# Kernel tuning notes

Measured on AMD Instinct MI355X. Metric: run time of the kernel, lower is better.

Reference implementation:

```python
import jax, jax.numpy as jnp
import numpy as np

G = 56          # voxel grid resolution per axis
N = 65536
K = 27          # 3x3x3 kernel offsets
C_IN = 128
C_OUT = 128


def _build_rulebook():
    """Submanifold conv rulebook: for each kernel offset, (input_row, output_row) pairs.

    Padded to P=N pairs per offset; invalid pairs use in_idx=0 and out_idx=N
    (a dummy output slot that is dropped), so shapes are static.
    """
    rng = np.random.default_rng(0)
    keys = np.sort(rng.choice(G ** 3, size=N, replace=False)).astype(np.int64)
    x = keys // (G * G)
    y = (keys // G) % G
    z = keys % G
    in_idx = np.zeros((K, N), dtype=np.int32)
    out_idx = np.full((K, N), N, dtype=np.int32)
    k = 0
    for dx in (-1, 0, 1):
        for dy in (-1, 0, 1):
            for dz in (-1, 0, 1):
                nx, ny, nz = x + dx, y + dy, z + dz
                valid = (nx >= 0) & (nx < G) & (ny >= 0) & (ny < G) & (nz >= 0) & (nz < G)
                nkey = (nx * G + ny) * G + nz
                pos = np.searchsorted(keys, np.clip(nkey, 0, G ** 3 - 1))
                pos = np.clip(pos, 0, N - 1)
                found = valid & (keys[pos] == nkey)
                cnt = int(found.sum())
                in_idx[k, :cnt] = pos[found]
                out_idx[k, :cnt] = np.nonzero(found)[0]
                k += 1
    return jnp.asarray(in_idx), jnp.asarray(out_idx)


def setup_inputs() -> dict:
    key = jax.random.key(0)
    k1, k2, k3 = jax.random.split(key, 3)
    fan_in = K * C_IN
    features = jax.random.normal(k1, (N, C_IN), dtype=jnp.float32)
    weight = jax.random.normal(k2, (K, C_IN, C_OUT), dtype=jnp.float32) * (1.0 / np.sqrt(fan_in))
    bias = jax.random.normal(k3, (C_OUT,), dtype=jnp.float32) * 0.01
    in_idx, out_idx = _build_rulebook()
    return {"features": features, "weight": weight, "bias": bias,
            "in_idx": in_idx, "out_idx": out_idx}


def reference(features, weight, bias, in_idx, out_idx):
    # gather: [K, P, C_in]
    gathered = features[in_idx]
    # per-offset GEMM: [K, P, C_out]
    contrib = jnp.einsum('kpc,kcd->kpd', gathered, weight)
    n = features.shape[0]
    c_out = weight.shape[-1]
    # scatter-accumulate into N real rows + 1 dummy row for padded pairs
    out = jnp.zeros((n + 1, c_out), dtype=features.dtype)
    out = out.at[out_idx.reshape(-1)].add(contrib.reshape(-1, c_out))
    return out[:n] + bias
```

## Files before the change

kernel.cpp:

```cpp
#include <hip/hip_runtime.h>
#include <hip/hip_bf16.h>
#include <stdint.h>

#define NV   65536
#define KOFF 27
#define CIN  128
#define COUT 128
#define NSEC (NV + 128)

typedef __bf16 bf16x8 __attribute__((ext_vector_type(8)));
typedef float  f32x4  __attribute__((ext_vector_type(4)));

__device__ __forceinline__ void async_copy16(void* lds, const void* g) {
    __builtin_amdgcn_global_load_lds(
        (const __attribute__((address_space(1))) void*)g,
        (__attribute__((address_space(3))) void*)lds,
        16, 0, 0);
}

#define JOB_A_BLOCKS 4097
#define JOB_B_BLOCKS 216
#define JOB_S_BLOCKS 1728

__global__ void k_prep_all(const float* __restrict__ f,
                           uint4* __restrict__ fb4,
                           const float* __restrict__ w,
                           uint4* __restrict__ wfrag4,
                           const int4* __restrict__ in4,
                           const int4* __restrict__ out4,
                           int* __restrict__ nbr) {
    const int b = blockIdx.x;
    const int t = threadIdx.x;
    if (b < JOB_A_BLOCKS) {
        int i = b * 256 + t;
        int total8  = (NV + 1) * CIN / 8;
        int nvalid8 = NV * CIN / 8;
        if (i >= total8) return;
        union { uint4 u; __hip_bfloat16 h[8]; } p;
        if (i < nvalid8) {
            const float4* f4 = (const float4*)f;
            float4 a = f4[i * 2];
            float4 c = f4[i * 2 + 1];
            p.h[0] = __float2bfloat16(a.x);
            p.h[1] = __float2bfloat16(a.y);
            p.h[2] = __float2bfloat16(a.z);
            p.h[3] = __float2bfloat16(a.w);
            p.h[4] = __float2bfloat16(c.x);
            p.h[5] = __float2bfloat16(c.y);
            p.h[6] = __float2bfloat16(c.z);
            p.h[7] = __float2bfloat16(c.w);
        } else {
            p.u = make_uint4(0, 0, 0, 0);
        }
        fb4[i] = p.u;
    } else if (b < JOB_A_BLOCKS + JOB_B_BLOCKS) {
        int c    = (b - JOB_A_BLOCKS) * 256 + t;
        int lane = c & 63;
        int nt   = (c >> 6) & 1;
        int ks   = (c >> 7) & 3;
        int wv   = (c >> 9) & 3;
        int k    = c >> 11;
        int cout = wv * 32 + nt * 16 + (lane & 15);
        int cin0 = ks * 32 + (lane >> 4) * 8;
        const float* wk = w + k * 16384;
        union { uint4 u; __hip_bfloat16 h[8]; } p;
        #pragma unroll
        for (int j = 0; j < 8; ++j)
            p.h[j] = __float2bfloat16(wk[(cin0 + j) * 128 + cout]);
        wfrag4[c] = p.u;
    } else {
        int i = (b - JOB_A_BLOCKS - JOB_B_BLOCKS) * 256 + t;
        int k = i >> 14;
        int4 ii = in4[i];
        int4 oo = out4[i];
        int* nb = nbr + (size_t)k * NSEC;
        auto POS = [](int o) {
            return (o >> 7) * 128 + (o & 15) * 8 + ((o >> 4) & 7);
        };
        nb[POS(oo.x)] = ii.x;
        nb[POS(oo.y)] = ii.y;
        nb[POS(oo.z)] = ii.z;
        nb[POS(oo.w)] = ii.w;
    }
}

__global__ __launch_bounds__(256, 2)
void sp_conv_main(const __hip_bfloat16* __restrict__ feats,
                  const uint4* __restrict__ wfrag,
                  const int* __restrict__ nbrt,
                  const float* __restrict__ bias,
                  float* __restrict__ out) {
    __shared__ unsigned char smem[65536];

    const int t   = threadIdx.x;
    const int bid = blockIdx.x;
    const int tile0 = ((bid & 7) * 64 + (bid >> 3)) * 128;

    const int w    = t >> 6;
    const int lane = t & 63;
    const int lr   = lane & 15;
    const int quad = lane >> 4;

    const int srow  = t >> 4;
    const int sbyte = ((t & 15) ^ srow) * 16;

    f32x4 acc[8][2] = {};

    const unsigned char* featsB = (const unsigned char*)feats;

    int  arows[8];
    uint4 bA[4][2], bB[4][2];

    auto NLOAD = [&](int k) {
        const int4* np = (const int4*)(nbrt + (size_t)k * NSEC + tile0 + srow * 8);
        int4 a0 = np[0];
        int4 a1 = np[1];
        arows[0] = a0.x; arows[1] = a0.y; arows[2] = a0.z; arows[3] = a0.w;
        arows[4] = a1.x; arows[5] = a1.y; arows[6] = a1.z; arows[7] = a1.w;
    };
    auto STAGE = [&](int sb) {
        #pragma unroll
        for (int i = 0; i < 8; ++i) {
            unsigned ar = min((unsigned)arows[i], (unsigned)NV);
            async_copy16(smem + sb + i * 4096 + t * 16,
                         featsB + (size_t)ar * 256 + sbyte);
        }
    };
    auto BLOAD = [&](const uint4* wfk, uint4 (&b)[4][2]) {
        #pragma unroll
        for (int ks = 0; ks < 4; ++ks)
            #pragma unroll
            for (int nt = 0; nt < 2; ++nt)
                b[ks][nt] = wfk[ks * 128 + nt * 64];
    };
    auto AFLOAD = [&](int rb, int ks, bf16x8 (&af)[8]) {
        #pragma unroll
        for (int mt = 0; mt < 8; ++mt)
            af[mt] = *(const bf16x8*)(smem + rb + (mt * 16 + lr) * 256 +
                                      (((ks * 4 + quad) ^ lr) * 16));
    };
    auto MFMA16 = [&](bf16x8 (&af)[8], uint4 (&b)[2]) {
        #pragma unroll
        for (int mt = 0; mt < 8; ++mt)
            #pragma unroll
            for (int nt = 0; nt < 2; ++nt)
                acc[mt][nt] = __builtin_amdgcn_mfma_f32_16x16x32_bf16(
                    af[mt], *(const bf16x8*)&b[nt], acc[mt][nt], 0, 0, 0);
    };

    NLOAD(0);
    STAGE(0);
    __builtin_amdgcn_sched_barrier(0);
    NLOAD(1);
    BLOAD(wfrag + w * 512 + lane, bA);
    asm volatile("s_waitcnt vmcnt(10)" ::: "memory");
    __builtin_amdgcn_s_barrier();
    __builtin_amdgcn_sched_barrier(0);

    auto ITER = [&](int k, int rb, uint4 (&buse)[4][2], uint4 (&bload)[4][2]) {
        STAGE(rb ^ 32768);
        __builtin_amdgcn_sched_barrier(0);
        NLOAD(min(k + 2, KOFF - 1));
        BLOAD(wfrag + (k + 1) * 2048 + w * 512 + lane, bload);
        #pragma unroll
        for (int ks = 0; ks < 4; ++ks) {
            bf16x8 af[8];
            AFLOAD(rb, ks, af);
            __builtin_amdgcn_s_setprio(1);
            MFMA16(af, buse[ks]);
            __builtin_amdgcn_s_setprio(0);
        }
        __builtin_amdgcn_sched_barrier(0);
        asm volatile("s_waitcnt vmcnt(10)" ::: "memory");
        __builtin_amdgcn_s_barrier();
        __builtin_amdgcn_sched_barrier(0);
    };

    #pragma unroll 1
    for (int kk = 0; kk < KOFF - 1; kk += 2) {
        ITER(kk,     0,     bA, bB);
        ITER(kk + 1, 32768, bB, bA);
    }

    #pragma unroll
    for (int ks = 0; ks < 4; ++ks) {
        bf16x8 af[8];
        AFLOAD(0, ks, af);
        MFMA16(af, bA[ks]);
    }

    const int n0w = w * 32;
    float bv[2];
    #pragma unroll
    for (int nt = 0; nt < 2; ++nt) bv[nt] = bias[n0w + nt * 16 + lr];

    #pragma unroll
    for (int mt = 0; mt < 8; ++mt) {
        #pragma unroll
        for (int nt = 0; nt < 2; ++nt) {
            #pragma unroll
            for (int r = 0; r < 4; ++r) {
                int grow = tile0 + mt * 16 + quad * 4 + r;
                out[(size_t)grow * COUT + n0w + nt * 16 + lr] =
                    acc[mt][nt][r] + bv[nt];
            }
        }
    }
}


extern "C" void kernel_launch(void* const* d_in, const int* in_sizes, int n_in,
                              void* d_out, int out_size, void* d_ws, size_t ws_size,
                              hipStream_t stream) {
    const float* features = (const float*)d_in[0];
    const float* weight   = (const float*)d_in[1];
    const float* bias     = (const float*)d_in[2];
    const int*   in_idx   = (const int*)d_in[3];
    const int*   out_idx  = (const int*)d_in[4];
    float* out = (float*)d_out;

    uint8_t* ws = (uint8_t*)d_ws;
    size_t off = 0;
    __hip_bfloat16* feats_bf = (__hip_bfloat16*)(ws + off);
    off += (size_t)(NV + 1) * CIN * 2;
    off = (off + 255) & ~(size_t)255;
    uint4* wfrag = (uint4*)(ws + off);
    off += (size_t)KOFF * CIN * COUT * 2;
    off = (off + 255) & ~(size_t)255;
    int* nbr = (int*)(ws + off);

    hipMemsetAsync(nbr, 0xFF, (size_t)KOFF * NSEC * 4, stream);

    k_prep_all<<<JOB_A_BLOCKS + JOB_B_BLOCKS + JOB_S_BLOCKS, 256, 0, stream>>>(
        features, (uint4*)feats_bf, weight, wfrag,
        (const int4*)in_idx, (const int4*)out_idx, nbr);

    sp_conv_main<<<NV / 128, 256, 0, stream>>>(feats_bf, wfrag, nbr, bias, out);
}
```

Before: 151.6 us.

## Switch warp tiling to 2x2 grid and stream weight fragments in halves

Each of the four waves now computes a 64x64 output sub-tile (2x2 wave grid) instead of a 128x32 strip, so each wave loads 4 A fragments and 4 B fragments per k-step. This halves the LDS A-fragment reads per wave while doubling the B fragments per wave. The double-buffered B registers are replaced by a single buffer that is refilled in two halves interleaved with the MFMA phases, cutting register pressure. This relies on the next offset's weight loads landing before they are consumed, and the vmcnt wait count is adjusted to match.

```diff
diff --git a/kernel.cpp b/kernel.cpp
--- a/kernel.cpp
+++ b/kernel.cpp
@@ -100,16 +100,18 @@
     const int lane = t & 63;
     const int lr   = lane & 15;
     const int quad = lane >> 4;
+    const int wr   = w >> 1;
+    const int wc   = w & 1;
 
     const int srow  = t >> 4;
     const int sbyte = ((t & 15) ^ srow) * 16;
 
-    f32x4 acc[8][2] = {};
+    f32x4 acc[4][4] = {};
 
     const unsigned char* featsB = (const unsigned char*)feats;
 
     int  arows[8];
-    uint4 bA[4][2], bB[4][2];
+    uint4 bcur[4][4];
 
     auto NLOAD = [&](int k) {
         const int4* np = (const int4*)(nbrt + (size_t)k * NSEC + tile0 + srow * 8);
@@ -126,24 +128,25 @@
                          featsB + (size_t)ar * 256 + sbyte);
         }
     };
-    auto BLOAD = [&](const uint4* wfk, uint4 (&b)[4][2]) {
-        #pragma unroll
-        for (int ks = 0; ks < 4; ++ks)
+    auto BLOAD2 = [&](const uint4* wfk, int ks0) {
+        #pragma unroll
+        for (int ks = 0; ks < 2; ++ks)
             #pragma unroll
-            for (int nt = 0; nt < 2; ++nt)
-                b[ks][nt] = wfk[ks * 128 + nt * 64];
-    };
-    auto AFLOAD = [&](int rb, int ks, bf16x8 (&af)[8]) {
-        #pragma unroll
-        for (int mt = 0; mt < 8; ++mt)
-            af[mt] = *(const bf16x8*)(smem + rb + (mt * 16 + lr) * 256 +
+            for (int nt = 0; nt < 4; ++nt)
+                bcur[ks0 + ks][nt] =
+                    wfk[(nt >> 1) * 512 + (nt & 1) * 64 + (ks0 + ks) * 128];
+    };
+    auto AFLOAD = [&](int rb, int ks, bf16x8 (&af)[4]) {
+        #pragma unroll
+        for (int mt = 0; mt < 4; ++mt)
+            af[mt] = *(const bf16x8*)(smem + rb + (wr * 64 + mt * 16 + lr) * 256 +
                                       (((ks * 4 + quad) ^ lr) * 16));
     };
-    auto MFMA16 = [&](bf16x8 (&af)[8], uint4 (&b)[2]) {
-        #pragma unroll
-        for (int mt = 0; mt < 8; ++mt)
+    auto MFMA16 = [&](bf16x8 (&af)[4], uint4 (&b)[4]) {
+        #pragma unroll
+        for (int mt = 0; mt < 4; ++mt)
             #pragma unroll
-            for (int nt = 0; nt < 2; ++nt)
+            for (int nt = 0; nt < 4; ++nt)
                 acc[mt][nt] = __builtin_amdgcn_mfma_f32_16x16x32_bf16(
                     af[mt], *(const bf16x8*)&b[nt], acc[mt][nt], 0, 0, 0);
     };
@@ -152,55 +155,73 @@
     STAGE(0);
     __builtin_amdgcn_sched_barrier(0);
     NLOAD(1);
-    BLOAD(wfrag + w * 512 + lane, bA);
-    asm volatile("s_waitcnt vmcnt(10)" ::: "memory");
+    {
+        const uint4* wf0 = wfrag + wc * 1024 + lane;
+        BLOAD2(wf0, 0);
+        BLOAD2(wf0, 2);
+    }
+    asm volatile("s_waitcnt vmcnt(18)" ::: "memory");
     __builtin_amdgcn_s_barrier();
     __builtin_amdgcn_sched_barrier(0);
 
-    auto ITER = [&](int k, int rb, uint4 (&buse)[4][2], uint4 (&bload)[4][2]) {
+    auto ITER = [&](int k, int rb) {
+        const uint4* wfn = wfrag + (min(k + 1, KOFF - 1)) * 2048 + wc * 1024 + lane;
         STAGE(rb ^ 32768);
         __builtin_amdgcn_sched_barrier(0);
         NLOAD(min(k + 2, KOFF - 1));
-        BLOAD(wfrag + (k + 1) * 2048 + w * 512 + lane, bload);
-        #pragma unroll
-        for (int ks = 0; ks < 4; ++ks) {
-            bf16x8 af[8];
+        __builtin_amdgcn_sched_barrier(0);
+        #pragma unroll
+        for (int ks = 0; ks < 2; ++ks) {
+            bf16x8 af[4];
             AFLOAD(rb, ks, af);
             __builtin_amdgcn_s_setprio(1);
-            MFMA16(af, buse[ks]);
+            MFMA16(af, bcur[ks]);
             __builtin_amdgcn_s_setprio(0);
         }
         __builtin_amdgcn_sched_barrier(0);
-        asm volatile("s_waitcnt vmcnt(10)" ::: "memory");
+        BLOAD2(wfn, 0);
+        __builtin_amdgcn_sched_barrier(0);
+        #pragma unroll
+        for (int ks = 2; ks < 4; ++ks) {
+            bf16x8 af[4];
+            AFLOAD(rb, ks, af);
+            __builtin_amdgcn_s_setprio(1);
+            MFMA16(af, bcur[ks]);
+            __builtin_amdgcn_s_setprio(0);
+        }
+        __builtin_amdgcn_sched_barrier(0);
+        BLOAD2(wfn, 2);
+        __builtin_amdgcn_sched_barrier(0);
+        asm volatile("s_waitcnt vmcnt(18)" ::: "memory");
         __builtin_amdgcn_s_barrier();
         __builtin_amdgcn_sched_barrier(0);
     };
 
     #pragma unroll 1
     for (int kk = 0; kk < KOFF - 1; kk += 2) {
-        ITER(kk,     0,     bA, bB);
-        ITER(kk + 1, 32768, bB, bA);
+        ITER(kk,     0);
+        ITER(kk + 1, 32768);
     }
 
     #pragma unroll
     for (int ks = 0; ks < 4; ++ks) {
-        bf16x8 af[8];
+        bf16x8 af[4];
         AFLOAD(0, ks, af);
-        MFMA16(af, bA[ks]);
-    }
-
-    const int n0w = w * 32;
-    float bv[2];
+        MFMA16(af, bcur[ks]);
+    }
+
+    const int n0w = wc * 64;
+    float bv[4];
     #pragma unroll
-    for (int nt = 0; nt < 2; ++nt) bv[nt] = bias[n0w + nt * 16 + lr];
+    for (int nt = 0; nt < 4; ++nt) bv[nt] = bias[n0w + nt * 16 + lr];
 
     #pragma unroll
-    for (int mt = 0; mt < 8; ++mt) {
-        #pragma unroll
-        for (int nt = 0; nt < 2; ++nt) {
+    for (int mt = 0; mt < 4; ++mt) {
+        #pragma unroll
+        for (int nt = 0; nt < 4; ++nt) {
             #pragma unroll
             for (int r = 0; r < 4; ++r) {
-                int grow = tile0 + mt * 16 + quad * 4 + r;
+                int grow = tile0 + wr * 64 + mt * 16 + quad * 4 + r;
                 out[(size_t)grow * COUT + n0w + nt * 16 + lr] =
                     acc[mt][nt][r] + bv[nt];
             }
```

Result: no change. 153.4 us (+1.2%).

## Add dedicated producer wavefront for async gather staging of feature rows

Applied to the files above, without the earlier changes.

Adds a fifth wavefront per block that loads the neighbor indices and issues all async global-to-LDS gathers for the next offset. The four compute wavefronts now only load weight fragments and run MFMAs, synchronising with the producer through block barriers. The neighbor table is now written in natural row order instead of a permuted order, and the LDS swizzle is moved into the producer's chunk XOR. The goal is to take gather-issue work and vmcnt waits off the MFMA waves, at the cost of a larger block, serialized readlane address generation in one wave, and a full vmcnt(0) wait each step.

```diff
diff --git a/kernel.cpp b/kernel.cpp
--- a/kernel.cpp
+++ b/kernel.cpp
@@ -74,20 +74,17 @@
         int4 ii = in4[i];
         int4 oo = out4[i];
         int* nb = nbr + (size_t)k * NSEC;
-        auto POS = [](int o) {
-            return (o >> 7) * 128 + (o & 15) * 8 + ((o >> 4) & 7);
-        };
-        nb[POS(oo.x)] = ii.x;
-        nb[POS(oo.y)] = ii.y;
-        nb[POS(oo.z)] = ii.z;
-        nb[POS(oo.w)] = ii.w;
-    }
-}
-
-__global__ __launch_bounds__(256, 2)
+        nb[oo.x] = ii.x;
+        nb[oo.y] = ii.y;
+        nb[oo.z] = ii.z;
+        nb[oo.w] = ii.w;
+    }
+}
+
+__global__ __launch_bounds__(320, 2)
 void sp_conv_main(const __hip_bfloat16* __restrict__ feats,
                   const uint4* __restrict__ wfrag,
-                  const int* __restrict__ nbrt,
+                  const int* __restrict__ nbrp,
                   const float* __restrict__ bias,
                   float* __restrict__ out) {
     __shared__ unsigned char smem[65536];
@@ -101,31 +98,49 @@
     const int lr   = lane & 15;
     const int quad = lane >> 4;
 
-    const int srow  = t >> 4;
-    const int sbyte = ((t & 15) ^ srow) * 16;
+    const unsigned char* featsB = (const unsigned char*)feats;
+
+    if (w == 4) {
+        auto NBRLOAD = [&](int k) {
+            int4 v = make_int4(NV, NV, NV, NV);
+            if (lane < 32)
+                v = *(const int4*)(nbrp + (size_t)k * NSEC + tile0 + lane * 4);
+            return v;
+        };
+        auto PSTAGE = [&](int sb, int4 nv) {
+            #pragma unroll
+            for (int j = 0; j < 32; ++j) {
+                unsigned r0 = min((unsigned)__builtin_amdgcn_readlane(nv.x, j), (unsigned)NV);
+                unsigned r1 = min((unsigned)__builtin_amdgcn_readlane(nv.y, j), (unsigned)NV);
+                unsigned r2 = min((unsigned)__builtin_amdgcn_readlane(nv.z, j), (unsigned)NV);
+                unsigned r3 = min((unsigned)__builtin_amdgcn_readlane(nv.w, j), (unsigned)NV);
+                unsigned ar = quad == 0 ? r0 : quad == 1 ? r1 : quad == 2 ? r2 : r3;
+                unsigned chunk = (unsigned)(lane & 15) ^ ((unsigned)(j & 3) * 4 + (unsigned)quad);
+                async_copy16(smem + sb + j * 1024 + lane * 16,
+                             featsB + (size_t)ar * 256 + chunk * 16);
+            }
+        };
+
+        int4 nvC = NBRLOAD(0);
+        int4 nvN = NBRLOAD(1);
+        PSTAGE(0, nvC);
+        asm volatile("s_waitcnt vmcnt(0)" ::: "memory");
+        __builtin_amdgcn_s_barrier();
+        nvC = nvN;
+        #pragma unroll 1
+        for (int k = 0; k < KOFF - 1; ++k) {
+            nvN = NBRLOAD(min(k + 2, KOFF - 1));
+            PSTAGE(((k + 1) & 1) * 32768, nvC);
+            asm volatile("s_waitcnt vmcnt(0)" ::: "memory");
+            __builtin_amdgcn_s_barrier();
+            nvC = nvN;
+        }
+        return;
+    }
 
     f32x4 acc[8][2] = {};
-
-    const unsigned char* featsB = (const unsigned char*)feats;
-
-    int  arows[8];
     uint4 bA[4][2], bB[4][2];
 
-    auto NLOAD = [&](int k) {
-        const int4* np = (const int4*)(nbrt + (size_t)k * NSEC + tile0 + srow * 8);
-        int4 a0 = np[0];
-        int4 a1 = np[1];
-        arows[0] = a0.x; arows[1] = a0.y; arows[2] = a0.z; arows[3] = a0.w;
-        arows[4] = a1.x; arows[5] = a1.y; arows[6] = a1.z; arows[7] = a1.w;
-    };
-    auto STAGE = [&](int sb) {
-        #pragma unroll
-        for (int i = 0; i < 8; ++i) {
-            unsigned ar = min((unsigned)arows[i], (unsigned)NV);
-            async_copy16(smem + sb + i * 4096 + t * 16,
-                         featsB + (size_t)ar * 256 + sbyte);
-        }
-    };
     auto BLOAD = [&](const uint4* wfk, uint4 (&b)[4][2]) {
         #pragma unroll
         for (int ks = 0; ks < 4; ++ks)
@@ -147,47 +162,28 @@
                 acc[mt][nt] = __builtin_amdgcn_mfma_f32_16x16x32_bf16(
                     af[mt], *(const bf16x8*)&b[nt], acc[mt][nt], 0, 0, 0);
     };
-
-    NLOAD(0);
-    STAGE(0);
-    __builtin_amdgcn_sched_barrier(0);
-    NLOAD(1);
-    BLOAD(wfrag + w * 512 + lane, bA);
-    asm volatile("s_waitcnt vmcnt(10)" ::: "memory");
-    __builtin_amdgcn_s_barrier();
-    __builtin_amdgcn_sched_barrier(0);
-
-    auto ITER = [&](int k, int rb, uint4 (&buse)[4][2], uint4 (&bload)[4][2]) {
-        STAGE(rb ^ 32768);
-        __builtin_amdgcn_sched_barrier(0);
-        NLOAD(min(k + 2, KOFF - 1));
-        BLOAD(wfrag + (k + 1) * 2048 + w * 512 + lane, bload);
+    auto COMPUTE = [&](int rb, uint4 (&buse)[4][2]) {
         #pragma unroll
         for (int ks = 0; ks < 4; ++ks) {
             bf16x8 af[8];
             AFLOAD(rb, ks, af);
-            __builtin_amdgcn_s_setprio(1);
             MFMA16(af, buse[ks]);
-            __builtin_amdgcn_s_setprio(0);
-        }
-        __builtin_amdgcn_sched_barrier(0);
-        asm volatile("s_waitcnt vmcnt(10)" ::: "memory");
-        __builtin_amdgcn_s_barrier();
-        __builtin_amdgcn_sched_barrier(0);
-    };
+        }
+    };
+
+    BLOAD(wfrag + w * 512 + lane, bA);
+    __builtin_amdgcn_s_barrier();
 
     #pragma unroll 1
     for (int kk = 0; kk < KOFF - 1; kk += 2) {
-        ITER(kk,     0,     bA, bB);
-        ITER(kk + 1, 32768, bB, bA);
-    }
-
-    #pragma unroll
-    for (int ks = 0; ks < 4; ++ks) {
-        bf16x8 af[8];
-        AFLOAD(0, ks, af);
-        MFMA16(af, bA[ks]);
-    }
+        BLOAD(wfrag + (kk + 1) * 2048 + w * 512 + lane, bB);
+        COMPUTE(0, bA);
+        __builtin_amdgcn_s_barrier();
+        BLOAD(wfrag + (kk + 2) * 2048 + w * 512 + lane, bA);
+        COMPUTE(32768, bB);
+        __builtin_amdgcn_s_barrier();
+    }
+    COMPUTE(0, bA);
 
     const int n0w = w * 32;
     float bv[2];
@@ -235,5 +231,5 @@
         features, (uint4*)feats_bf, weight, wfrag,
         (const int4*)in_idx, (const int4*)out_idx, nbr);
 
-    sp_conv_main<<<NV / 128, 256, 0, stream>>>(feats_bf, wfrag, nbr, bias, out);
-}
+    sp_conv_main<<<NV / 128, 320, 0, stream>>>(feats_bf, wfrag, nbr, bias, out);
+}
```

New measurement: 256.2 us. +69.0%, slower.

## Switch to 32x32x16 MFMA with 2x2 wave tiling and single weight buffer

Applied to the files above, without the earlier changes.

Replaces the 16x16x32 bf16 MFMA with 32x32x16 MFMA. The four waves now split the 128x128 tile 2x2 (64 rows by 64 cols each) instead of 128 rows by 32 cols per wave, so each wave reads a quarter of the A tile from LDS. The weight fragment layout in the prep kernel is rearranged to match. The double-buffered weight registers become one buffer refilled slice by slice right after each use, which cuts register pressure but can leave MFMAs waiting on global loads.

```diff
diff --git a/kernel.cpp b/kernel.cpp
--- a/kernel.cpp
+++ b/kernel.cpp
@@ -9,7 +9,7 @@
 #define NSEC (NV + 128)
 
 typedef __bf16 bf16x8 __attribute__((ext_vector_type(8)));
-typedef float  f32x4  __attribute__((ext_vector_type(4)));
+typedef float  f32x16 __attribute__((ext_vector_type(16)));
 
 __device__ __forceinline__ void async_copy16(void* lds, const void* g) {
     __builtin_amdgcn_global_load_lds(
@@ -56,12 +56,12 @@
     } else if (b < JOB_A_BLOCKS + JOB_B_BLOCKS) {
         int c    = (b - JOB_A_BLOCKS) * 256 + t;
         int lane = c & 63;
-        int nt   = (c >> 6) & 1;
-        int ks   = (c >> 7) & 3;
-        int wv   = (c >> 9) & 3;
+        int ks   = (c >> 6) & 7;
+        int nb   = (c >> 9) & 1;
+        int wc   = (c >> 10) & 1;
         int k    = c >> 11;
-        int cout = wv * 32 + nt * 16 + (lane & 15);
-        int cin0 = ks * 32 + (lane >> 4) * 8;
+        int cout = wc * 64 + nb * 32 + (lane & 31);
+        int cin0 = ks * 16 + (lane >> 5) * 8;
         const float* wk = w + k * 16384;
         union { uint4 u; __hip_bfloat16 h[8]; } p;
         #pragma unroll
@@ -98,18 +98,23 @@
 
     const int w    = t >> 6;
     const int lane = t & 63;
-    const int lr   = lane & 15;
-    const int quad = lane >> 4;
+    const int wr   = w >> 1;
+    const int wc   = w & 1;
+    const int l31  = lane & 31;
+    const int part = lane >> 5;
+    const int x15  = lane & 15;
 
     const int srow  = t >> 4;
     const int sbyte = ((t & 15) ^ srow) * 16;
 
-    f32x4 acc[8][2] = {};
+    const int rowb0 = (wr * 64 + l31) * 256;
+    const int rowb1 = rowb0 + 8192;
+
+    f32x16 acc[2][2] = {};
+    uint4  bcur[8][2];
 
     const unsigned char* featsB = (const unsigned char*)feats;
-
-    int  arows[8];
-    uint4 bA[4][2], bB[4][2];
+    int arows[8];
 
     auto NLOAD = [&](int k) {
         const int4* np = (const int4*)(nbrt + (size_t)k * NSEC + tile0 + srow * 8);
@@ -126,83 +131,84 @@
                          featsB + (size_t)ar * 256 + sbyte);
         }
     };
-    auto BLOAD = [&](const uint4* wfk, uint4 (&b)[4][2]) {
-        #pragma unroll
-        for (int ks = 0; ks < 4; ++ks)
-            #pragma unroll
-            for (int nt = 0; nt < 2; ++nt)
-                b[ks][nt] = wfk[ks * 128 + nt * 64];
-    };
-    auto AFLOAD = [&](int rb, int ks, bf16x8 (&af)[8]) {
-        #pragma unroll
-        for (int mt = 0; mt < 8; ++mt)
-            af[mt] = *(const bf16x8*)(smem + rb + (mt * 16 + lr) * 256 +
-                                      (((ks * 4 + quad) ^ lr) * 16));
-    };
-    auto MFMA16 = [&](bf16x8 (&af)[8], uint4 (&b)[2]) {
-        #pragma unroll
-        for (int mt = 0; mt < 8; ++mt)
-            #pragma unroll
-            for (int nt = 0; nt < 2; ++nt)
-                acc[mt][nt] = __builtin_amdgcn_mfma_f32_16x16x32_bf16(
-                    af[mt], *(const bf16x8*)&b[nt], acc[mt][nt], 0, 0, 0);
-    };
 
     NLOAD(0);
     STAGE(0);
     __builtin_amdgcn_sched_barrier(0);
     NLOAD(1);
-    BLOAD(wfrag + w * 512 + lane, bA);
-    asm volatile("s_waitcnt vmcnt(10)" ::: "memory");
+    {
+        const uint4* wf0 = wfrag + wc * 1024 + lane;
+        #pragma unroll
+        for (int ks = 0; ks < 8; ++ks) {
+            bcur[ks][0] = wf0[ks * 64];
+            bcur[ks][1] = wf0[ks * 64 + 512];
+        }
+    }
+    asm volatile("s_waitcnt vmcnt(18)" ::: "memory");
     __builtin_amdgcn_s_barrier();
     __builtin_amdgcn_sched_barrier(0);
 
-    auto ITER = [&](int k, int rb, uint4 (&buse)[4][2], uint4 (&bload)[4][2]) {
+    auto ITER = [&](int k, int rb) {
         STAGE(rb ^ 32768);
         __builtin_amdgcn_sched_barrier(0);
         NLOAD(min(k + 2, KOFF - 1));
-        BLOAD(wfrag + (k + 1) * 2048 + w * 512 + lane, bload);
-        #pragma unroll
-        for (int ks = 0; ks < 4; ++ks) {
-            bf16x8 af[8];
-            AFLOAD(rb, ks, af);
-            __builtin_amdgcn_s_setprio(1);
-            MFMA16(af, buse[ks]);
-            __builtin_amdgcn_s_setprio(0);
-        }
-        __builtin_amdgcn_sched_barrier(0);
-        asm volatile("s_waitcnt vmcnt(10)" ::: "memory");
+        const uint4* wfn = wfrag + (k + 1) * 2048 + wc * 1024 + lane;
+        #pragma unroll
+        for (int ks = 0; ks < 8; ++ks) {
+            bf16x8 af0 = *(const bf16x8*)(smem + rb + rowb0 +
+                                          (((ks * 2 + part) ^ x15) << 4));
+            bf16x8 af1 = *(const bf16x8*)(smem + rb + rowb1 +
+                                          (((ks * 2 + part) ^ x15) << 4));
+            acc[0][0] = __builtin_amdgcn_mfma_f32_32x32x16_bf16(
+                af0, *(const bf16x8*)&bcur[ks][0], acc[0][0], 0, 0, 0);
+            acc[0][1] = __builtin_amdgcn_mfma_f32_32x32x16_bf16(
+                af0, *(const bf16x8*)&bcur[ks][1], acc[0][1], 0, 0, 0);
+            acc[1][0] = __builtin_amdgcn_mfma_f32_32x32x16_bf16(
+                af1, *(const bf16x8*)&bcur[ks][0], acc[1][0], 0, 0, 0);
+            acc[1][1] = __builtin_amdgcn_mfma_f32_32x32x16_bf16(
+                af1, *(const bf16x8*)&bcur[ks][1], acc[1][1], 0, 0, 0);
+            bcur[ks][0] = wfn[ks * 64];
+            bcur[ks][1] = wfn[ks * 64 + 512];
+        }
+        asm volatile("s_waitcnt vmcnt(18)" ::: "memory");
         __builtin_amdgcn_s_barrier();
         __builtin_amdgcn_sched_barrier(0);
     };
 
     #pragma unroll 1
     for (int kk = 0; kk < KOFF - 1; kk += 2) {
-        ITER(kk,     0,     bA, bB);
-        ITER(kk + 1, 32768, bB, bA);
+        ITER(kk,     0);
+        ITER(kk + 1, 32768);
     }
 
     #pragma unroll
-    for (int ks = 0; ks < 4; ++ks) {
-        bf16x8 af[8];
-        AFLOAD(0, ks, af);
-        MFMA16(af, bA[ks]);
-    }
-
-    const int n0w = w * 32;
+    for (int ks = 0; ks < 8; ++ks) {
+        bf16x8 af0 = *(const bf16x8*)(smem + rowb0 + (((ks * 2 + part) ^ x15) << 4));
+        bf16x8 af1 = *(const bf16x8*)(smem + rowb1 + (((ks * 2 + part) ^ x15) << 4));
+        acc[0][0] = __builtin_amdgcn_mfma_f32_32x32x16_bf16(
+            af0, *(const bf16x8*)&bcur[ks][0], acc[0][0], 0, 0, 0);
+        acc[0][1] = __builtin_amdgcn_mfma_f32_32x32x16_bf16(
+            af0, *(const bf16x8*)&bcur[ks][1], acc[0][1], 0, 0, 0);
+        acc[1][0] = __builtin_amdgcn_mfma_f32_32x32x16_bf16(
+            af1, *(const bf16x8*)&bcur[ks][0], acc[1][0], 0, 0, 0);
+        acc[1][1] = __builtin_amdgcn_mfma_f32_32x32x16_bf16(
+            af1, *(const bf16x8*)&bcur[ks][1], acc[1][1], 0, 0, 0);
+    }
+
     float bv[2];
     #pragma unroll
-    for (int nt = 0; nt < 2; ++nt) bv[nt] = bias[n0w + nt * 16 + lr];
+    for (int nb = 0; nb < 2; ++nb) bv[nb] = bias[wc * 64 + nb * 32 + l31];
 
     #pragma unroll
-    for (int mt = 0; mt < 8; ++mt) {
-        #pragma unroll
-        for (int nt = 0; nt < 2; ++nt) {
+    for (int mr = 0; mr < 2; ++mr) {
+        #pragma unroll
+        for (int nb = 0; nb < 2; ++nb) {
             #pragma unroll
-            for (int r = 0; r < 4; ++r) {
-                int grow = tile0 + mt * 16 + quad * 4 + r;
-                out[(size_t)grow * COUT + n0w + nt * 16 + lr] =
-                    acc[mt][nt][r] + bv[nt];
+            for (int r = 0; r < 16; ++r) {
+                int grow = tile0 + wr * 64 + mr * 32 +
+                           (r & 3) + 8 * (r >> 2) + 4 * part;
+                int gcol = wc * 64 + nb * 32 + l31;
+                out[(size_t)grow * COUT + gcol] = acc[mr][nb][r] + bv[nb];
             }
         }
     }
```

Result: slower. 160.3 us (+5.7%).
